# Optimization experiments

Hardware: AMD Instinct MI355X
Metric: run time of the kernel (lower is better)

Reference implementation:

```python
import jax, jax.numpy as jnp
import numpy as np

D_MODEL = 1024
N_HEADS = 16
D_K = D_MODEL // N_HEADS


def setup_inputs() -> dict:
    key = jax.random.key(0)
    ks = jax.random.split(key, 10)
    B, S = 4, 2048
    std = 1.0 / np.sqrt(D_MODEL)
    inp = {
        "x": jax.random.normal(ks[0], (B, S, D_MODEL), dtype=jnp.float32),
        "attention_mask": jnp.ones((B, S), dtype=jnp.int32),
        "W_q": jax.random.normal(ks[1], (D_MODEL, D_MODEL), dtype=jnp.float32) * std,
        "b_q": jnp.zeros((D_MODEL,), dtype=jnp.float32),
        "W_k": jax.random.normal(ks[2], (D_MODEL, D_MODEL), dtype=jnp.float32) * std,
        "b_k": jnp.zeros((D_MODEL,), dtype=jnp.float32),
        "W_v": jax.random.normal(ks[3], (D_MODEL, D_MODEL), dtype=jnp.float32) * std,
        "b_v": jnp.zeros((D_MODEL,), dtype=jnp.float32),
        "W_o": jax.random.normal(ks[4], (D_MODEL, D_MODEL), dtype=jnp.float32) * std,
        "b_o": jnp.zeros((D_MODEL,), dtype=jnp.float32),
    }
    return inp


def reference(x, attention_mask, W_q, b_q, W_k, b_k, W_v, b_v, W_o, b_o):
    B, S, _ = x.shape
    # projections -> [B, H, S, d_k]
    def proj(W, b):
        return (x @ W.T + b).reshape(B, S, N_HEADS, D_K).transpose(0, 2, 1, 3)
    q = proj(W_q, b_q)
    k = proj(W_k, b_k)
    v = proj(W_v, b_v)
    scores = jnp.einsum("bhqd,bhkd->bhqk", q, k) / jnp.sqrt(jnp.float32(D_K))
    mask = attention_mask[:, None, None, :] == 0  # [B,1,1,S]
    scores = jnp.where(mask, -jnp.inf, scores)
    probs = jax.nn.softmax(scores, axis=-1)  # dropout p=0 (eval)
    out = jnp.einsum("bhqk,bhkd->bhqd", probs, v)
    out = out.transpose(0, 2, 1, 3).reshape(B, S, D_MODEL)
    return out @ W_o.T + b_o
```

## Files before the change

### kernel.cpp

```cpp
#include <hip/hip_runtime.h>
#include <hip/hip_bf16.h>


#define SEQ   2048
#define DM    1024
#define NH    16
#define DK    64
#define MTOT  8192

typedef unsigned short u16;
typedef __attribute__((ext_vector_type(8))) short bf16x8;
typedef __attribute__((ext_vector_type(4))) float f32x4;

typedef union { unsigned u[4]; bf16x8 v; } FragU;

#define MFMA(a, b, c) __builtin_amdgcn_mfma_f32_16x16x32_bf16((a), (b), (c), 0, 0, 0)

#if __has_builtin(__builtin_amdgcn_exp2f)
#define EXP2(x) __builtin_amdgcn_exp2f(x)
#else
#define EXP2(x) __expf((x) * 0.69314718056f)
#endif

__device__ __forceinline__ u16 f2bf(float v) {
    unsigned int x = __float_as_uint(v);
    x += 0x7fffu + ((x >> 16) & 1u);
    return (u16)(x >> 16);
}
__device__ __forceinline__ float bf2f(u16 u) {
    return __uint_as_float(((unsigned int)u) << 16);
}
__device__ __forceinline__ unsigned pk2bf(float a, float b) {
    __hip_bfloat162 t = __float22bfloat162_rn(make_float2(a, b));
    unsigned r;
    __builtin_memcpy(&r, &t, 4);
    return r;
}

__device__ __forceinline__ void gl_lds16(const void* g, void* l) {
    __builtin_amdgcn_global_load_lds((__attribute__((address_space(1))) void*)g,
                                     (__attribute__((address_space(3))) void*)l,
                                     16, 0, 0);
}

__global__ __launch_bounds__(256) void split_f32(const float* __restrict__ src,
                                                 u16* __restrict__ dh,
                                                 u16* __restrict__ dl, int n4) {
    int i = blockIdx.x * 256 + threadIdx.x;
    if (i >= n4) return;
    float4 v = ((const float4*)src)[i];
    const float* f = (const float*)&v;
    ushort4 hh, ll;
    u16* hp = (u16*)&hh;
    u16* lp = (u16*)&ll;
#pragma unroll
    for (int j = 0; j < 4; ++j) {
        u16 h = f2bf(f[j]);
        hp[j] = h;
        lp[j] = f2bf(f[j] - bf2f(h));
    }
    ((ushort4*)dh)[i] = hh;
    ((ushort4*)dl)[i] = ll;
}

template <int MODE>
__global__ __launch_bounds__(256, 2) void gemm_split(
    const u16* __restrict__ Ah, const u16* __restrict__ Al,
    const u16* __restrict__ Bh, const u16* __restrict__ Bl,
    const float* __restrict__ bias,
    float* __restrict__ outF, u16* __restrict__ outH, u16* __restrict__ outL) {
    __shared__ u16 sm[4][128 * 64];

    const int tid = threadIdx.x;
    const int w = tid >> 6, lane = tid & 63;
    const int n0 = blockIdx.x * 128, m0 = blockIdx.y * 128;
    const int wr = w >> 1, wc = w & 1;
    const int rowoff = lane >> 3;
    const int cswz = ((lane & 7) ^ rowoff) << 3;

    const u16* src = (w == 0) ? Ah : (w == 1) ? Al : (w == 2) ? Bh : Bl;
    const int row0 = (w < 2) ? m0 : n0;
    const u16* sbase = src + (size_t)(row0 + rowoff) * 1024 + cswz;

    f32x4 acc[4][4];
#pragma unroll
    for (int a = 0; a < 4; ++a)
#pragma unroll
        for (int b = 0; b < 4; ++b) acc[a][b] = (f32x4)0.f;

    for (int k0 = 0; k0 < 1024; k0 += 64) {
#pragma unroll
        for (int i = 0; i < 16; ++i)
            gl_lds16(sbase + (size_t)(8 * i) * 1024 + k0, &sm[w][i * 512]);
        __syncthreads();
#pragma unroll
        for (int kk = 0; kk < 2; ++kk) {
            bf16x8 ah[4], al[4], bh[4], bl[4];
#pragma unroll
            for (int t = 0; t < 4; ++t) {
                const int Ra = wr * 64 + t * 16 + (lane & 15);
                const int oa = Ra * 128 + ((((kk << 2) + (lane >> 4)) ^ (Ra & 7)) << 4);
                ah[t] = *(const bf16x8*)((const char*)&sm[0][0] + oa);
                al[t] = *(const bf16x8*)((const char*)&sm[1][0] + oa);
                const int Rb = wc * 64 + t * 16 + (lane & 15);
                const int ob = Rb * 128 + ((((kk << 2) + (lane >> 4)) ^ (Rb & 7)) << 4);
                bh[t] = *(const bf16x8*)((const char*)&sm[2][0] + ob);
                bl[t] = *(const bf16x8*)((const char*)&sm[3][0] + ob);
            }
#pragma unroll
            for (int mt = 0; mt < 4; ++mt)
#pragma unroll
                for (int nt = 0; nt < 4; ++nt) {
                    acc[mt][nt] = MFMA(ah[mt], bh[nt], acc[mt][nt]);
                    acc[mt][nt] = MFMA(ah[mt], bl[nt], acc[mt][nt]);
                    acc[mt][nt] = MFMA(al[mt], bh[nt], acc[mt][nt]);
                }
        }
        __syncthreads();
    }

#pragma unroll
    for (int mt = 0; mt < 4; ++mt) {
#pragma unroll
        for (int nt = 0; nt < 4; ++nt) {
            const int n = n0 + wc * 64 + nt * 16 + (lane & 15);
            const float bv = bias[n];
#pragma unroll
            for (int j = 0; j < 4; ++j) {
                const int m = m0 + wr * 64 + mt * 16 + (lane >> 4) * 4 + j;
                const float v = acc[mt][nt][j] + bv;
                if (MODE == 0) {
                    outF[(size_t)m * 1024 + n] = v;
                } else {
                    const u16 h16 = f2bf(v);
                    const u16 l16 = f2bf(v - bf2f(h16));
                    const int b = m >> 11, s = m & 2047, hh = n >> 6, dk = n & 63;
                    size_t idx;
                    if (MODE == 1) idx = (((size_t)(b * 16 + hh)) * 2048 + s) * 64 + dk;
                    else           idx = (((size_t)(b * 16 + hh)) * 64 + dk) * 2048 + s;
                    outH[idx] = h16;
                    outL[idx] = l16;
                }
            }
        }
    }
}

__global__ __launch_bounds__(256, 4) void flash_mfma2(
    const u16* __restrict__ Qh, const u16* __restrict__ Ql,
    const u16* __restrict__ Kh, const u16* __restrict__ Kl,
    const u16* __restrict__ Vh, const u16* __restrict__ Vl,
    const int* __restrict__ amask,
    u16* __restrict__ Ch, u16* __restrict__ Cl) {
    __shared__ u16 sK[2][64 * 64];
    __shared__ u16 sV[2][64 * 64];
    __shared__ unsigned sMask[64];

    const int tid = threadIdx.x, w = tid >> 6, lane = tid & 63;
    const int qt = blockIdx.x, bh = blockIdx.y;
    const int b = bh >> 4, h = bh & 15;
    const int q0 = qt * 64;
    const int hi = lane >> 4, l15 = lane & 15;
    const int rowoff = lane >> 3;
    const int cswz = ((lane & 7) ^ rowoff) << 3;
    const size_t kvbase = (size_t)bh * 2048;
    const float CE = 0.125f * 1.44269504089f;

    {
        const int* ap = amask + b * 2048 + tid * 8;
        int4 a0 = *(const int4*)ap;
        int4 a1 = *(const int4*)(ap + 4);
        unsigned byte = (unsigned)(a0.x != 0) | ((unsigned)(a0.y != 0) << 1) |
                        ((unsigned)(a0.z != 0) << 2) | ((unsigned)(a0.w != 0) << 3) |
                        ((unsigned)(a1.x != 0) << 4) | ((unsigned)(a1.y != 0) << 5) |
                        ((unsigned)(a1.z != 0) << 6) | ((unsigned)(a1.w != 0) << 7);
        ((unsigned char*)sMask)[tid] = (unsigned char)byte;
    }

    bf16x8 qfh[2], qfl[2];
    {
        const size_t qrow = kvbase + q0 + w * 16 + l15;
        const int koff = hi * 8;
#pragma unroll
        for (int kk = 0; kk < 2; ++kk) {
            qfh[kk] = *(const bf16x8*)(Qh + qrow * 64 + kk * 32 + koff);
            qfl[kk] = *(const bf16x8*)(Ql + qrow * 64 + kk * 32 + koff);
        }
    }

    f32x4 o[4];
#pragma unroll
    for (int d = 0; d < 4; ++d) o[d] = (f32x4)0.f;
    float mi = -1e30f, li = 0.f;

    for (int kt = 0; kt < SEQ / 64; ++kt) {
        const int k0 = kt * 64;
        __syncthreads();
        {
            const u16* src = (w == 0) ? Kh : (w == 1) ? Kl : (w == 2) ? Vh : Vl;
            u16* dst = (w == 0) ? &sK[0][0] : (w == 1) ? &sK[1][0]
                     : (w == 2) ? &sV[0][0] : &sV[1][0];
            if (w < 2) {
                const u16* sb = src + (kvbase + k0 + rowoff) * 64 + cswz;
#pragma unroll
                for (int i = 0; i < 8; ++i)
                    gl_lds16(sb + (size_t)(8 * i) * 64, dst + i * 512);
            } else {
                const u16* sb = src + ((size_t)bh * 64 + rowoff) * 2048 + k0 + cswz;
#pragma unroll
                for (int i = 0; i < 8; ++i)
                    gl_lds16(sb + (size_t)(8 * i) * 2048, dst + i * 512);
            }
        }
        __syncthreads();

        f32x4 s[4];
#pragma unroll
        for (int nt = 0; nt < 4; ++nt) s[nt] = (f32x4)0.f;
#pragma unroll
        for (int kk = 0; kk < 2; ++kk)
#pragma unroll
            for (int nt = 0; nt < 4; ++nt) {
                const int Rb = nt * 16 + l15;
                const int ob = Rb * 128 + ((((kk << 2) + hi) ^ (Rb & 7)) << 4);
                bf16x8 kbh = *(const bf16x8*)((const char*)&sK[0][0] + ob);
                bf16x8 kbl = *(const bf16x8*)((const char*)&sK[1][0] + ob);
                s[nt] = MFMA(kbh, qfh[kk], s[nt]);
                s[nt] = MFMA(kbh, qfl[kk], s[nt]);
                s[nt] = MFMA(kbl, qfh[kk], s[nt]);
            }

        const unsigned mlo = sMask[2 * kt], mhw = sMask[2 * kt + 1];
        if ((mlo & mhw) != 0xFFFFFFFFu) {
#pragma unroll
            for (int nt = 0; nt < 4; ++nt) {
                const unsigned mw = (nt & 2) ? mhw : mlo;
                const unsigned bits = mw >> (((nt & 1) << 4) + (hi << 2));
#pragma unroll
                for (int j = 0; j < 4; ++j)
                    if (!((bits >> j) & 1u)) s[nt][j] = -2e30f;
            }
        }

        float pm = s[0][0];
#pragma unroll
        for (int nt = 0; nt < 4; ++nt)
#pragma unroll
            for (int j = 0; j < 4; ++j) pm = fmaxf(pm, s[nt][j]);
        pm = fmaxf(pm, __shfl_xor(pm, 16));
        pm = fmaxf(pm, __shfl_xor(pm, 32));
        if (__any(pm > mi + 64.f)) {
            const float mnew = fmaxf(mi, pm);
            const float sc = EXP2((mi - mnew) * CE);
            li *= sc;
#pragma unroll
            for (int d = 0; d < 4; ++d) o[d] *= sc;
            mi = mnew;
        }
        const float nm = -mi * CE;
        float p[4][4];
        float rs = 0.f;
#pragma unroll
        for (int nt = 0; nt < 4; ++nt)
#pragma unroll
            for (int j = 0; j < 4; ++j) {
                const float e = EXP2(fmaf(s[nt][j], CE, nm));
                p[nt][j] = e;
                rs += e;
            }
        rs += __shfl_xor(rs, 16);
        rs += __shfl_xor(rs, 32);
        li += rs;

        unsigned qph[4][2], qpl[4][2];
#pragma unroll
        for (int nt = 0; nt < 4; ++nt)
#pragma unroll
            for (int c = 0; c < 2; ++c) {
                const float v0 = p[nt][2 * c], v1 = p[nt][2 * c + 1];
                const unsigned wh = pk2bf(v0, v1);
                qph[nt][c] = wh;
                const float r0 = v0 - __uint_as_float(wh << 16);
                const float r1 = v1 - __uint_as_float(wh & 0xffff0000u);
                qpl[nt][c] = pk2bf(r0, r1);
            }

        const int src01 = l15 | ((lane & 16) << 1);
        const int src23 = src01 + 16;
#pragma unroll
        for (int kkv = 0; kkv < 2; ++kkv) {
            const unsigned ah0 = __shfl(qph[2 * kkv][0], src01);
            const unsigned ah1 = __shfl(qph[2 * kkv][1], src01);
            const unsigned ah2 = __shfl(qph[2 * kkv][0], src23);
            const unsigned ah3 = __shfl(qph[2 * kkv][1], src23);
            const unsigned bh0 = __shfl(qph[2 * kkv + 1][0], src01);
            const unsigned bh1 = __shfl(qph[2 * kkv + 1][1], src01);
            const unsigned bh2 = __shfl(qph[2 * kkv + 1][0], src23);
            const unsigned bh3 = __shfl(qph[2 * kkv + 1][1], src23);
            const unsigned al0 = __shfl(qpl[2 * kkv][0], src01);
            const unsigned al1 = __shfl(qpl[2 * kkv][1], src01);
            const unsigned al2 = __shfl(qpl[2 * kkv][0], src23);
            const unsigned al3 = __shfl(qpl[2 * kkv][1], src23);
            const unsigned bl0 = __shfl(qpl[2 * kkv + 1][0], src01);
            const unsigned bl1 = __shfl(qpl[2 * kkv + 1][1], src01);
            const unsigned bl2 = __shfl(qpl[2 * kkv + 1][0], src23);
            const unsigned bl3 = __shfl(qpl[2 * kkv + 1][1], src23);
            const bool up = (hi >= 2);
            FragU uh, ul;
            uh.u[0] = up ? bh0 : ah0;
            uh.u[1] = up ? bh1 : ah1;
            uh.u[2] = up ? bh2 : ah2;
            uh.u[3] = up ? bh3 : ah3;
            ul.u[0] = up ? bl0 : al0;
            ul.u[1] = up ? bl1 : al1;
            ul.u[2] = up ? bl2 : al2;
            ul.u[3] = up ? bl3 : al3;
            const bf16x8 pbh = uh.v, pbl = ul.v;
#pragma unroll
            for (int ntd = 0; ntd < 4; ++ntd) {
                const int Rv = ntd * 16 + l15;
                const int ov = Rv * 128 + ((((kkv << 2) + hi) ^ (Rv & 7)) << 4);
                bf16x8 vbh = *(const bf16x8*)((const char*)&sV[0][0] + ov);
                bf16x8 vbl = *(const bf16x8*)((const char*)&sV[1][0] + ov);
                o[ntd] = MFMA(vbh, pbh, o[ntd]);
                o[ntd] = MFMA(vbh, pbl, o[ntd]);
                o[ntd] = MFMA(vbl, pbh, o[ntd]);
            }
        }
    }

    const float inv = 1.f / li;
    const int srow = q0 + w * 16 + l15;
    const size_t obase = ((size_t)b * 2048 + srow) * 1024 + h * 64;
#pragma unroll
    for (int ntd = 0; ntd < 4; ++ntd) {
        const float v0 = o[ntd][0] * inv, v1 = o[ntd][1] * inv;
        const float v2 = o[ntd][2] * inv, v3 = o[ntd][3] * inv;
        const unsigned wh0 = pk2bf(v0, v1), wh1 = pk2bf(v2, v3);
        const float r0 = v0 - __uint_as_float(wh0 << 16);
        const float r1 = v1 - __uint_as_float(wh0 & 0xffff0000u);
        const float r2 = v2 - __uint_as_float(wh1 << 16);
        const float r3 = v3 - __uint_as_float(wh1 & 0xffff0000u);
        const unsigned wl0 = pk2bf(r0, r1), wl1 = pk2bf(r2, r3);
        const size_t idx = obase + ntd * 16 + hi * 4;
        uint2 sh, sl;
        sh.x = wh0; sh.y = wh1;
        sl.x = wl0; sl.y = wl1;
        *(uint2*)&Ch[idx] = sh;
        *(uint2*)&Cl[idx] = sl;
    }
}

extern "C" void kernel_launch(void* const* d_in, const int* in_sizes, int n_in,
                              void* d_out, int out_size, void* d_ws, size_t ws_size,
                              hipStream_t stream) {
    const float* x  = (const float*)d_in[0];
    const int* am   = (const int*)d_in[1];
    const float* Wq = (const float*)d_in[2];
    const float* bq = (const float*)d_in[3];
    const float* Wk = (const float*)d_in[4];
    const float* bk = (const float*)d_in[5];
    const float* Wv = (const float*)d_in[6];
    const float* bv = (const float*)d_in[7];
    const float* Wo = (const float*)d_in[8];
    const float* bo = (const float*)d_in[9];
    float* out = (float*)d_out;

    const size_t MB = 1u << 20;
    char* ws = (char*)d_ws;
    u16* Xh  = (u16*)(ws + 0 * MB);
    u16* Xl  = (u16*)(ws + 16 * MB);
    u16* qh  = (u16*)(ws + 32 * MB);
    u16* ql  = (u16*)(ws + 48 * MB);
    u16* kh  = (u16*)(ws + 64 * MB);
    u16* kl  = (u16*)(ws + 80 * MB);
    u16* vh  = (u16*)(ws + 96 * MB);
    u16* vl  = (u16*)(ws + 112 * MB);
    u16* Wqh = (u16*)(ws + 128 * MB);
    u16* Wql = (u16*)(ws + 130 * MB);
    u16* Wkh = (u16*)(ws + 132 * MB);
    u16* Wkl = (u16*)(ws + 134 * MB);
    u16* Wvh = (u16*)(ws + 136 * MB);
    u16* Wvl = (u16*)(ws + 138 * MB);
    u16* Woh = (u16*)(ws + 140 * MB);
    u16* Wol = (u16*)(ws + 142 * MB);

    split_f32<<<(MTOT * DM / 4 + 255) / 256, 256, 0, stream>>>(x, Xh, Xl, MTOT * DM / 4);
    split_f32<<<(DM * DM / 4 + 255) / 256, 256, 0, stream>>>(Wq, Wqh, Wql, DM * DM / 4);
    split_f32<<<(DM * DM / 4 + 255) / 256, 256, 0, stream>>>(Wk, Wkh, Wkl, DM * DM / 4);
    split_f32<<<(DM * DM / 4 + 255) / 256, 256, 0, stream>>>(Wv, Wvh, Wvl, DM * DM / 4);
    split_f32<<<(DM * DM / 4 + 255) / 256, 256, 0, stream>>>(Wo, Woh, Wol, DM * DM / 4);

    dim3 ggrid(DM / 128, MTOT / 128);
    gemm_split<1><<<ggrid, 256, 0, stream>>>(Xh, Xl, Wqh, Wql, bq, nullptr, qh, ql);
    gemm_split<1><<<ggrid, 256, 0, stream>>>(Xh, Xl, Wkh, Wkl, bk, nullptr, kh, kl);
    gemm_split<2><<<ggrid, 256, 0, stream>>>(Xh, Xl, Wvh, Wvl, bv, nullptr, vh, vl);

    flash_mfma2<<<dim3(SEQ / 64, 4 * NH), 256, 0, stream>>>(qh, ql, kh, kl, vh, vl, am, Xh, Xl);

    gemm_split<0><<<ggrid, 256, 0, stream>>>(Xh, Xl, Woh, Wol, bo, out, nullptr, nullptr);
}
```

Before: 590.6 us.

## Fuse QKV projections into one launch and double flash query tile

The three Q/K/V projection GEMMs become a single launch with a 24-wide grid, where the block's x index picks the weight set, bias and output layout. This removes launch gaps and fills the GPU with a bigger grid. The flash attention kernel now uses 512 threads (8 waves) per block covering 128 queries, so each K/V tile in shared memory serves twice as many queries and global loads are split across twice as many waves. The risk is lower occupancy or register pressure under the new launch bounds, and fewer blocks (1024) for attention.

```diff
diff --git a/kernel.cpp b/kernel.cpp
--- a/kernel.cpp
+++ b/kernel.cpp
@@ -63,20 +63,35 @@
     ((ushort4*)dl)[i] = ll;
 }
 
-template <int MODE>
-__global__ __launch_bounds__(256, 2) void gemm_split(
+__global__ __launch_bounds__(256, 2) void gemm_qkv(
     const u16* __restrict__ Ah, const u16* __restrict__ Al,
-    const u16* __restrict__ Bh, const u16* __restrict__ Bl,
-    const float* __restrict__ bias,
-    float* __restrict__ outF, u16* __restrict__ outH, u16* __restrict__ outL) {
+    const u16* __restrict__ Wqh, const u16* __restrict__ Wql,
+    const u16* __restrict__ Wkh, const u16* __restrict__ Wkl,
+    const u16* __restrict__ Wvh, const u16* __restrict__ Wvl,
+    const float* __restrict__ bq, const float* __restrict__ bk,
+    const float* __restrict__ bv,
+    u16* __restrict__ qh, u16* __restrict__ ql,
+    u16* __restrict__ kh, u16* __restrict__ kl,
+    u16* __restrict__ vh, u16* __restrict__ vl) {
     __shared__ u16 sm[4][128 * 64];
 
     const int tid = threadIdx.x;
     const int w = tid >> 6, lane = tid & 63;
-    const int n0 = blockIdx.x * 128, m0 = blockIdx.y * 128;
+    const int bx = blockIdx.x;
+    const int sel = bx >> 3;
+    const int n0 = (bx & 7) * 128, m0 = blockIdx.y * 128;
     const int wr = w >> 1, wc = w & 1;
     const int rowoff = lane >> 3;
     const int cswz = ((lane & 7) ^ rowoff) << 3;
+
+    const u16* Bh;
+    const u16* Bl;
+    const float* bias;
+    u16* oH;
+    u16* oL;
+    if (sel == 0)      { Bh = Wqh; Bl = Wql; bias = bq; oH = qh; oL = ql; }
+    else if (sel == 1) { Bh = Wkh; Bl = Wkl; bias = bk; oH = kh; oL = kl; }
+    else               { Bh = Wvh; Bl = Wvl; bias = bv; oH = vh; oL = vl; }
 
     const u16* src = (w == 0) ? Ah : (w == 1) ? Al : (w == 2) ? Bh : Bl;
     const int row0 = (w < 2) ? m0 : n0;
@@ -124,29 +139,94 @@
 #pragma unroll
         for (int nt = 0; nt < 4; ++nt) {
             const int n = n0 + wc * 64 + nt * 16 + (lane & 15);
-            const float bv = bias[n];
+            const float bvv = bias[n];
 #pragma unroll
             for (int j = 0; j < 4; ++j) {
                 const int m = m0 + wr * 64 + mt * 16 + (lane >> 4) * 4 + j;
-                const float v = acc[mt][nt][j] + bv;
-                if (MODE == 0) {
-                    outF[(size_t)m * 1024 + n] = v;
-                } else {
-                    const u16 h16 = f2bf(v);
-                    const u16 l16 = f2bf(v - bf2f(h16));
-                    const int b = m >> 11, s = m & 2047, hh = n >> 6, dk = n & 63;
-                    size_t idx;
-                    if (MODE == 1) idx = (((size_t)(b * 16 + hh)) * 2048 + s) * 64 + dk;
-                    else           idx = (((size_t)(b * 16 + hh)) * 64 + dk) * 2048 + s;
-                    outH[idx] = h16;
-                    outL[idx] = l16;
+                const float v = acc[mt][nt][j] + bvv;
+                const u16 h16 = f2bf(v);
+                const u16 l16 = f2bf(v - bf2f(h16));
+                const int b = m >> 11, s = m & 2047, hh = n >> 6, dk = n & 63;
+                size_t idx;
+                if (sel != 2) idx = (((size_t)(b * 16 + hh)) * 2048 + s) * 64 + dk;
+                else          idx = (((size_t)(b * 16 + hh)) * 64 + dk) * 2048 + s;
+                oH[idx] = h16;
+                oL[idx] = l16;
+            }
+        }
+    }
+}
+
+__global__ __launch_bounds__(256, 2) void gemm_out(
+    const u16* __restrict__ Ah, const u16* __restrict__ Al,
+    const u16* __restrict__ Bh, const u16* __restrict__ Bl,
+    const float* __restrict__ bias, float* __restrict__ outF) {
+    __shared__ u16 sm[4][128 * 64];
+
+    const int tid = threadIdx.x;
+    const int w = tid >> 6, lane = tid & 63;
+    const int n0 = blockIdx.x * 128, m0 = blockIdx.y * 128;
+    const int wr = w >> 1, wc = w & 1;
+    const int rowoff = lane >> 3;
+    const int cswz = ((lane & 7) ^ rowoff) << 3;
+
+    const u16* src = (w == 0) ? Ah : (w == 1) ? Al : (w == 2) ? Bh : Bl;
+    const int row0 = (w < 2) ? m0 : n0;
+    const u16* sbase = src + (size_t)(row0 + rowoff) * 1024 + cswz;
+
+    f32x4 acc[4][4];
+#pragma unroll
+    for (int a = 0; a < 4; ++a)
+#pragma unroll
+        for (int b = 0; b < 4; ++b) acc[a][b] = (f32x4)0.f;
+
+    for (int k0 = 0; k0 < 1024; k0 += 64) {
+#pragma unroll
+        for (int i = 0; i < 16; ++i)
+            gl_lds16(sbase + (size_t)(8 * i) * 1024 + k0, &sm[w][i * 512]);
+        __syncthreads();
+#pragma unroll
+        for (int kk = 0; kk < 2; ++kk) {
+            bf16x8 ah[4], al[4], bh[4], bl[4];
+#pragma unroll
+            for (int t = 0; t < 4; ++t) {
+                const int Ra = wr * 64 + t * 16 + (lane & 15);
+                const int oa = Ra * 128 + ((((kk << 2) + (lane >> 4)) ^ (Ra & 7)) << 4);
+                ah[t] = *(const bf16x8*)((const char*)&sm[0][0] + oa);
+                al[t] = *(const bf16x8*)((const char*)&sm[1][0] + oa);
+                const int Rb = wc * 64 + t * 16 + (lane & 15);
+                const int ob = Rb * 128 + ((((kk << 2) + (lane >> 4)) ^ (Rb & 7)) << 4);
+                bh[t] = *(const bf16x8*)((const char*)&sm[2][0] + ob);
+                bl[t] = *(const bf16x8*)((const char*)&sm[3][0] + ob);
+            }
+#pragma unroll
+            for (int mt = 0; mt < 4; ++mt)
+#pragma unroll
+                for (int nt = 0; nt < 4; ++nt) {
+                    acc[mt][nt] = MFMA(ah[mt], bh[nt], acc[mt][nt]);
+                    acc[mt][nt] = MFMA(ah[mt], bl[nt], acc[mt][nt]);
+                    acc[mt][nt] = MFMA(al[mt], bh[nt], acc[mt][nt]);
                 }
-            }
-        }
-    }
-}
-
-__global__ __launch_bounds__(256, 4) void flash_mfma2(
+        }
+        __syncthreads();
+    }
+
+#pragma unroll
+    for (int mt = 0; mt < 4; ++mt) {
+#pragma unroll
+        for (int nt = 0; nt < 4; ++nt) {
+            const int n = n0 + wc * 64 + nt * 16 + (lane & 15);
+            const float bv = bias[n];
+#pragma unroll
+            for (int j = 0; j < 4; ++j) {
+                const int m = m0 + wr * 64 + mt * 16 + (lane >> 4) * 4 + j;
+                outF[(size_t)m * 1024 + n] = acc[mt][nt][j] + bv;
+            }
+        }
+    }
+}
+
+__global__ __launch_bounds__(512, 8) void flash_mfma3(
     const u16* __restrict__ Qh, const u16* __restrict__ Ql,
     const u16* __restrict__ Kh, const u16* __restrict__ Kl,
     const u16* __restrict__ Vh, const u16* __restrict__ Vl,
@@ -159,14 +239,14 @@
     const int tid = threadIdx.x, w = tid >> 6, lane = tid & 63;
     const int qt = blockIdx.x, bh = blockIdx.y;
     const int b = bh >> 4, h = bh & 15;
-    const int q0 = qt * 64;
+    const int q0 = qt * 128;
     const int hi = lane >> 4, l15 = lane & 15;
     const int rowoff = lane >> 3;
     const int cswz = ((lane & 7) ^ rowoff) << 3;
     const size_t kvbase = (size_t)bh * 2048;
     const float CE = 0.125f * 1.44269504089f;
 
-    {
+    if (tid < 256) {
         const int* ap = amask + b * 2048 + tid * 8;
         int4 a0 = *(const int4*)ap;
         int4 a1 = *(const int4*)(ap + 4);
@@ -188,6 +268,12 @@
         }
     }
 
+    const int arr = w >> 1;
+    const int c0 = (w & 1) * 4;
+    const u16* ssrc = (arr == 0) ? Kh : (arr == 1) ? Kl : (arr == 2) ? Vh : Vl;
+    u16* sdst = (arr == 0) ? &sK[0][0] : (arr == 1) ? &sK[1][0]
+              : (arr == 2) ? &sV[0][0] : &sV[1][0];
+
     f32x4 o[4];
 #pragma unroll
     for (int d = 0; d < 4; ++d) o[d] = (f32x4)0.f;
@@ -196,21 +282,16 @@
     for (int kt = 0; kt < SEQ / 64; ++kt) {
         const int k0 = kt * 64;
         __syncthreads();
-        {
-            const u16* src = (w == 0) ? Kh : (w == 1) ? Kl : (w == 2) ? Vh : Vl;
-            u16* dst = (w == 0) ? &sK[0][0] : (w == 1) ? &sK[1][0]
-                     : (w == 2) ? &sV[0][0] : &sV[1][0];
-            if (w < 2) {
-                const u16* sb = src + (kvbase + k0 + rowoff) * 64 + cswz;
-#pragma unroll
-                for (int i = 0; i < 8; ++i)
-                    gl_lds16(sb + (size_t)(8 * i) * 64, dst + i * 512);
-            } else {
-                const u16* sb = src + ((size_t)bh * 64 + rowoff) * 2048 + k0 + cswz;
-#pragma unroll
-                for (int i = 0; i < 8; ++i)
-                    gl_lds16(sb + (size_t)(8 * i) * 2048, dst + i * 512);
-            }
+        if (arr < 2) {
+            const u16* sb = ssrc + (kvbase + k0 + 8 * c0 + rowoff) * 64 + cswz;
+#pragma unroll
+            for (int i = 0; i < 4; ++i)
+                gl_lds16(sb + (size_t)(8 * i) * 64, sdst + (c0 + i) * 512);
+        } else {
+            const u16* sb = ssrc + ((size_t)bh * 64 + 8 * c0 + rowoff) * 2048 + k0 + cswz;
+#pragma unroll
+            for (int i = 0; i < 4; ++i)
+                gl_lds16(sb + (size_t)(8 * i) * 2048, sdst + (c0 + i) * 512);
         }
         __syncthreads();
 
@@ -391,12 +472,11 @@
     split_f32<<<(DM * DM / 4 + 255) / 256, 256, 0, stream>>>(Wv, Wvh, Wvl, DM * DM / 4);
     split_f32<<<(DM * DM / 4 + 255) / 256, 256, 0, stream>>>(Wo, Woh, Wol, DM * DM / 4);
 
-    dim3 ggrid(DM / 128, MTOT / 128);
-    gemm_split<1><<<ggrid, 256, 0, stream>>>(Xh, Xl, Wqh, Wql, bq, nullptr, qh, ql);
-    gemm_split<1><<<ggrid, 256, 0, stream>>>(Xh, Xl, Wkh, Wkl, bk, nullptr, kh, kl);
-    gemm_split<2><<<ggrid, 256, 0, stream>>>(Xh, Xl, Wvh, Wvl, bv, nullptr, vh, vl);
-
-    flash_mfma2<<<dim3(SEQ / 64, 4 * NH), 256, 0, stream>>>(qh, ql, kh, kl, vh, vl, am, Xh, Xl);
-
-    gemm_split<0><<<ggrid, 256, 0, stream>>>(Xh, Xl, Woh, Wol, bo, out, nullptr, nullptr);
-}
+    gemm_qkv<<<dim3(24, MTOT / 128), 256, 0, stream>>>(
+        Xh, Xl, Wqh, Wql, Wkh, Wkl, Wvh, Wvl, bq, bk, bv,
+        qh, ql, kh, kl, vh, vl);
+
+    flash_mfma3<<<dim3(SEQ / 128, 4 * NH), 512, 0, stream>>>(qh, ql, kh, kl, vh, vl, am, Xh, Xl);
+
+    gemm_out<<<dim3(DM / 128, MTOT / 128), 256, 0, stream>>>(Xh, Xl, Woh, Wol, bo, out);
+}
```

After: 645.5 us. 9.3% more time.

## Process two query subtiles per wave and remap blocks for XCD locality

Applied to the files above, without the earlier changes.

The flash attention kernel now handles 128 query rows per block, with each wave owning two 16-row subtiles. Each K/V tile loaded into LDS and each fragment read from LDS is therefore reused across twice as many MFMAs, halving K/V global and LDS traffic per query. The block index is also remapped so that all query tiles of a head land on the same XCD, which should improve L2 reuse of K/V. In exchange the kernel uses more registers (launch bounds drop to 2 blocks) and launches half as many blocks, which lowers occupancy and latency hiding.

```diff
diff --git a/kernel.cpp b/kernel.cpp
--- a/kernel.cpp
+++ b/kernel.cpp
@@ -146,7 +146,7 @@
     }
 }
 
-__global__ __launch_bounds__(256, 4) void flash_mfma2(
+__global__ __launch_bounds__(256, 2) void flash_mfma4(
     const u16* __restrict__ Qh, const u16* __restrict__ Ql,
     const u16* __restrict__ Kh, const u16* __restrict__ Kl,
     const u16* __restrict__ Vh, const u16* __restrict__ Vl,
@@ -157,9 +157,12 @@
     __shared__ unsigned sMask[64];
 
     const int tid = threadIdx.x, w = tid >> 6, lane = tid & 63;
-    const int qt = blockIdx.x, bh = blockIdx.y;
+    const int i_flat = blockIdx.x + 16 * blockIdx.y;
+    const int xcd = i_flat & 7, j_rem = i_flat >> 3;
+    const int bh = xcd * 8 + (j_rem >> 4);
+    const int qt = j_rem & 15;
     const int b = bh >> 4, h = bh & 15;
-    const int q0 = qt * 64;
+    const int q0 = qt * 128;
     const int hi = lane >> 4, l15 = lane & 15;
     const int rowoff = lane >> 3;
     const int cswz = ((lane & 7) ^ rowoff) << 3;
@@ -177,21 +180,27 @@
         ((unsigned char*)sMask)[tid] = (unsigned char)byte;
     }
 
-    bf16x8 qfh[2], qfl[2];
-    {
-        const size_t qrow = kvbase + q0 + w * 16 + l15;
+    bf16x8 qfh[2][2], qfl[2][2];
+#pragma unroll
+    for (int st = 0; st < 2; ++st) {
+        const size_t qrow = kvbase + q0 + w * 32 + st * 16 + l15;
         const int koff = hi * 8;
 #pragma unroll
         for (int kk = 0; kk < 2; ++kk) {
-            qfh[kk] = *(const bf16x8*)(Qh + qrow * 64 + kk * 32 + koff);
-            qfl[kk] = *(const bf16x8*)(Ql + qrow * 64 + kk * 32 + koff);
-        }
-    }
-
-    f32x4 o[4];
-#pragma unroll
-    for (int d = 0; d < 4; ++d) o[d] = (f32x4)0.f;
-    float mi = -1e30f, li = 0.f;
+            qfh[st][kk] = *(const bf16x8*)(Qh + qrow * 64 + kk * 32 + koff);
+            qfl[st][kk] = *(const bf16x8*)(Ql + qrow * 64 + kk * 32 + koff);
+        }
+    }
+
+    f32x4 o[2][4];
+    float mi[2], li[2];
+#pragma unroll
+    for (int st = 0; st < 2; ++st) {
+        mi[st] = -1e30f;
+        li[st] = 0.f;
+#pragma unroll
+        for (int d = 0; d < 4; ++d) o[st][d] = (f32x4)0.f;
+    }
 
     for (int kt = 0; kt < SEQ / 64; ++kt) {
         const int k0 = kt * 64;
@@ -214,9 +223,11 @@
         }
         __syncthreads();
 
-        f32x4 s[4];
-#pragma unroll
-        for (int nt = 0; nt < 4; ++nt) s[nt] = (f32x4)0.f;
+        f32x4 s[2][4];
+#pragma unroll
+        for (int st = 0; st < 2; ++st)
+#pragma unroll
+            for (int nt = 0; nt < 4; ++nt) s[st][nt] = (f32x4)0.f;
 #pragma unroll
         for (int kk = 0; kk < 2; ++kk)
 #pragma unroll
@@ -225,9 +236,12 @@
                 const int ob = Rb * 128 + ((((kk << 2) + hi) ^ (Rb & 7)) << 4);
                 bf16x8 kbh = *(const bf16x8*)((const char*)&sK[0][0] + ob);
                 bf16x8 kbl = *(const bf16x8*)((const char*)&sK[1][0] + ob);
-                s[nt] = MFMA(kbh, qfh[kk], s[nt]);
-                s[nt] = MFMA(kbh, qfl[kk], s[nt]);
-                s[nt] = MFMA(kbl, qfh[kk], s[nt]);
+                s[0][nt] = MFMA(kbh, qfh[0][kk], s[0][nt]);
+                s[0][nt] = MFMA(kbh, qfl[0][kk], s[0][nt]);
+                s[0][nt] = MFMA(kbl, qfh[0][kk], s[0][nt]);
+                s[1][nt] = MFMA(kbh, qfh[1][kk], s[1][nt]);
+                s[1][nt] = MFMA(kbh, qfl[1][kk], s[1][nt]);
+                s[1][nt] = MFMA(kbl, qfh[1][kk], s[1][nt]);
             }
 
         const unsigned mlo = sMask[2 * kt], mhw = sMask[2 * kt + 1];
@@ -238,116 +252,133 @@
                 const unsigned bits = mw >> (((nt & 1) << 4) + (hi << 2));
 #pragma unroll
                 for (int j = 0; j < 4; ++j)
-                    if (!((bits >> j) & 1u)) s[nt][j] = -2e30f;
-            }
-        }
-
-        float pm = s[0][0];
-#pragma unroll
-        for (int nt = 0; nt < 4; ++nt)
-#pragma unroll
-            for (int j = 0; j < 4; ++j) pm = fmaxf(pm, s[nt][j]);
-        pm = fmaxf(pm, __shfl_xor(pm, 16));
-        pm = fmaxf(pm, __shfl_xor(pm, 32));
-        if (__any(pm > mi + 64.f)) {
-            const float mnew = fmaxf(mi, pm);
-            const float sc = EXP2((mi - mnew) * CE);
-            li *= sc;
-#pragma unroll
-            for (int d = 0; d < 4; ++d) o[d] *= sc;
-            mi = mnew;
-        }
-        const float nm = -mi * CE;
-        float p[4][4];
-        float rs = 0.f;
-#pragma unroll
-        for (int nt = 0; nt < 4; ++nt)
-#pragma unroll
-            for (int j = 0; j < 4; ++j) {
-                const float e = EXP2(fmaf(s[nt][j], CE, nm));
-                p[nt][j] = e;
-                rs += e;
-            }
-        rs += __shfl_xor(rs, 16);
-        rs += __shfl_xor(rs, 32);
-        li += rs;
-
-        unsigned qph[4][2], qpl[4][2];
-#pragma unroll
-        for (int nt = 0; nt < 4; ++nt)
-#pragma unroll
-            for (int c = 0; c < 2; ++c) {
-                const float v0 = p[nt][2 * c], v1 = p[nt][2 * c + 1];
-                const unsigned wh = pk2bf(v0, v1);
-                qph[nt][c] = wh;
-                const float r0 = v0 - __uint_as_float(wh << 16);
-                const float r1 = v1 - __uint_as_float(wh & 0xffff0000u);
-                qpl[nt][c] = pk2bf(r0, r1);
-            }
+                    if (!((bits >> j) & 1u)) {
+                        s[0][nt][j] = -2e30f;
+                        s[1][nt][j] = -2e30f;
+                    }
+            }
+        }
+
+        unsigned qph[2][4][2], qpl[2][4][2];
+#pragma unroll
+        for (int st = 0; st < 2; ++st) {
+            float pm = s[st][0][0];
+#pragma unroll
+            for (int nt = 0; nt < 4; ++nt)
+#pragma unroll
+                for (int j = 0; j < 4; ++j) pm = fmaxf(pm, s[st][nt][j]);
+            pm = fmaxf(pm, __shfl_xor(pm, 16));
+            pm = fmaxf(pm, __shfl_xor(pm, 32));
+            if (__any(pm > mi[st] + 64.f)) {
+                const float mnew = fmaxf(mi[st], pm);
+                const float sc = EXP2((mi[st] - mnew) * CE);
+                li[st] *= sc;
+#pragma unroll
+                for (int d = 0; d < 4; ++d) o[st][d] *= sc;
+                mi[st] = mnew;
+            }
+            const float nm = -mi[st] * CE;
+            float p[4][4];
+            float rs = 0.f;
+#pragma unroll
+            for (int nt = 0; nt < 4; ++nt)
+#pragma unroll
+                for (int j = 0; j < 4; ++j) {
+                    const float e = EXP2(fmaf(s[st][nt][j], CE, nm));
+                    p[nt][j] = e;
+                    rs += e;
+                }
+            rs += __shfl_xor(rs, 16);
+            rs += __shfl_xor(rs, 32);
+            li[st] += rs;
+
+#pragma unroll
+            for (int nt = 0; nt < 4; ++nt)
+#pragma unroll
+                for (int c = 0; c < 2; ++c) {
+                    const float v0 = p[nt][2 * c], v1 = p[nt][2 * c + 1];
+                    const unsigned wh = pk2bf(v0, v1);
+                    qph[st][nt][c] = wh;
+                    const float r0 = v0 - __uint_as_float(wh << 16);
+                    const float r1 = v1 - __uint_as_float(wh & 0xffff0000u);
+                    qpl[st][nt][c] = pk2bf(r0, r1);
+                }
+        }
 
         const int src01 = l15 | ((lane & 16) << 1);
         const int src23 = src01 + 16;
 #pragma unroll
         for (int kkv = 0; kkv < 2; ++kkv) {
-            const unsigned ah0 = __shfl(qph[2 * kkv][0], src01);
-            const unsigned ah1 = __shfl(qph[2 * kkv][1], src01);
-            const unsigned ah2 = __shfl(qph[2 * kkv][0], src23);
-            const unsigned ah3 = __shfl(qph[2 * kkv][1], src23);
-            const unsigned bh0 = __shfl(qph[2 * kkv + 1][0], src01);
-            const unsigned bh1 = __shfl(qph[2 * kkv + 1][1], src01);
-            const unsigned bh2 = __shfl(qph[2 * kkv + 1][0], src23);
-            const unsigned bh3 = __shfl(qph[2 * kkv + 1][1], src23);
-            const unsigned al0 = __shfl(qpl[2 * kkv][0], src01);
-            const unsigned al1 = __shfl(qpl[2 * kkv][1], src01);
-            const unsigned al2 = __shfl(qpl[2 * kkv][0], src23);
-            const unsigned al3 = __shfl(qpl[2 * kkv][1], src23);
-            const unsigned bl0 = __shfl(qpl[2 * kkv + 1][0], src01);
-            const unsigned bl1 = __shfl(qpl[2 * kkv + 1][1], src01);
-            const unsigned bl2 = __shfl(qpl[2 * kkv + 1][0], src23);
-            const unsigned bl3 = __shfl(qpl[2 * kkv + 1][1], src23);
-            const bool up = (hi >= 2);
-            FragU uh, ul;
-            uh.u[0] = up ? bh0 : ah0;
-            uh.u[1] = up ? bh1 : ah1;
-            uh.u[2] = up ? bh2 : ah2;
-            uh.u[3] = up ? bh3 : ah3;
-            ul.u[0] = up ? bl0 : al0;
-            ul.u[1] = up ? bl1 : al1;
-            ul.u[2] = up ? bl2 : al2;
-            ul.u[3] = up ? bl3 : al3;
-            const bf16x8 pbh = uh.v, pbl = ul.v;
+            bf16x8 pbh[2], pbl[2];
+#pragma unroll
+            for (int st = 0; st < 2; ++st) {
+                const unsigned ah0 = __shfl(qph[st][2 * kkv][0], src01);
+                const unsigned ah1 = __shfl(qph[st][2 * kkv][1], src01);
+                const unsigned ah2 = __shfl(qph[st][2 * kkv][0], src23);
+                const unsigned ah3 = __shfl(qph[st][2 * kkv][1], src23);
+                const unsigned bh0 = __shfl(qph[st][2 * kkv + 1][0], src01);
+                const unsigned bh1 = __shfl(qph[st][2 * kkv + 1][1], src01);
+                const unsigned bh2 = __shfl(qph[st][2 * kkv + 1][0], src23);
+                const unsigned bh3 = __shfl(qph[st][2 * kkv + 1][1], src23);
+                const unsigned al0 = __shfl(qpl[st][2 * kkv][0], src01);
+                const unsigned al1 = __shfl(qpl[st][2 * kkv][1], src01);
+                const unsigned al2 = __shfl(qpl[st][2 * kkv][0], src23);
+                const unsigned al3 = __shfl(qpl[st][2 * kkv][1], src23);
+                const unsigned bl0 = __shfl(qpl[st][2 * kkv + 1][0], src01);
+                const unsigned bl1 = __shfl(qpl[st][2 * kkv + 1][1], src01);
+                const unsigned bl2 = __shfl(qpl[st][2 * kkv + 1][0], src23);
+                const unsigned bl3 = __shfl(qpl[st][2 * kkv + 1][1], src23);
+                const bool up = (hi >= 2);
+                FragU uh, ul;
+                uh.u[0] = up ? bh0 : ah0;
+                uh.u[1] = up ? bh1 : ah1;
+                uh.u[2] = up ? bh2 : ah2;
+                uh.u[3] = up ? bh3 : ah3;
+                ul.u[0] = up ? bl0 : al0;
+                ul.u[1] = up ? bl1 : al1;
+                ul.u[2] = up ? bl2 : al2;
+                ul.u[3] = up ? bl3 : al3;
+                pbh[st] = uh.v;
+                pbl[st] = ul.v;
+            }
 #pragma unroll
             for (int ntd = 0; ntd < 4; ++ntd) {
                 const int Rv = ntd * 16 + l15;
                 const int ov = Rv * 128 + ((((kkv << 2) + hi) ^ (Rv & 7)) << 4);
                 bf16x8 vbh = *(const bf16x8*)((const char*)&sV[0][0] + ov);
                 bf16x8 vbl = *(const bf16x8*)((const char*)&sV[1][0] + ov);
-                o[ntd] = MFMA(vbh, pbh, o[ntd]);
-                o[ntd] = MFMA(vbh, pbl, o[ntd]);
-                o[ntd] = MFMA(vbl, pbh, o[ntd]);
-            }
-        }
-    }
-
-    const float inv = 1.f / li;
-    const int srow = q0 + w * 16 + l15;
-    const size_t obase = ((size_t)b * 2048 + srow) * 1024 + h * 64;
-#pragma unroll
-    for (int ntd = 0; ntd < 4; ++ntd) {
-        const float v0 = o[ntd][0] * inv, v1 = o[ntd][1] * inv;
-        const float v2 = o[ntd][2] * inv, v3 = o[ntd][3] * inv;
-        const unsigned wh0 = pk2bf(v0, v1), wh1 = pk2bf(v2, v3);
-        const float r0 = v0 - __uint_as_float(wh0 << 16);
-        const float r1 = v1 - __uint_as_float(wh0 & 0xffff0000u);
-        const float r2 = v2 - __uint_as_float(wh1 << 16);
-        const float r3 = v3 - __uint_as_float(wh1 & 0xffff0000u);
-        const unsigned wl0 = pk2bf(r0, r1), wl1 = pk2bf(r2, r3);
-        const size_t idx = obase + ntd * 16 + hi * 4;
-        uint2 sh, sl;
-        sh.x = wh0; sh.y = wh1;
-        sl.x = wl0; sl.y = wl1;
-        *(uint2*)&Ch[idx] = sh;
-        *(uint2*)&Cl[idx] = sl;
+                o[0][ntd] = MFMA(vbh, pbh[0], o[0][ntd]);
+                o[0][ntd] = MFMA(vbh, pbl[0], o[0][ntd]);
+                o[0][ntd] = MFMA(vbl, pbh[0], o[0][ntd]);
+                o[1][ntd] = MFMA(vbh, pbh[1], o[1][ntd]);
+                o[1][ntd] = MFMA(vbh, pbl[1], o[1][ntd]);
+                o[1][ntd] = MFMA(vbl, pbh[1], o[1][ntd]);
+            }
+        }
+    }
+
+#pragma unroll
+    for (int st = 0; st < 2; ++st) {
+        const float inv = 1.f / li[st];
+        const int srow = q0 + w * 32 + st * 16 + l15;
+        const size_t obase = ((size_t)b * 2048 + srow) * 1024 + h * 64;
+#pragma unroll
+        for (int ntd = 0; ntd < 4; ++ntd) {
+            const float v0 = o[st][ntd][0] * inv, v1 = o[st][ntd][1] * inv;
+            const float v2 = o[st][ntd][2] * inv, v3 = o[st][ntd][3] * inv;
+            const unsigned wh0 = pk2bf(v0, v1), wh1 = pk2bf(v2, v3);
+            const float r0 = v0 - __uint_as_float(wh0 << 16);
+            const float r1 = v1 - __uint_as_float(wh0 & 0xffff0000u);
+            const float r2 = v2 - __uint_as_float(wh1 << 16);
+            const float r3 = v3 - __uint_as_float(wh1 & 0xffff0000u);
+            const unsigned wl0 = pk2bf(r0, r1), wl1 = pk2bf(r2, r3);
+            const size_t idx = obase + ntd * 16 + hi * 4;
+            uint2 sh, sl;
+            sh.x = wh0; sh.y = wh1;
+            sl.x = wl0; sl.y = wl1;
+            *(uint2*)&Ch[idx] = sh;
+            *(uint2*)&Cl[idx] = sl;
+        }
     }
 }
 
@@ -396,7 +427,7 @@
     gemm_split<1><<<ggrid, 256, 0, stream>>>(Xh, Xl, Wkh, Wkl, bk, nullptr, kh, kl);
     gemm_split<2><<<ggrid, 256, 0, stream>>>(Xh, Xl, Wvh, Wvl, bv, nullptr, vh, vl);
 
-    flash_mfma2<<<dim3(SEQ / 64, 4 * NH), 256, 0, stream>>>(qh, ql, kh, kl, vh, vl, am, Xh, Xl);
+    flash_mfma4<<<dim3(SEQ / 128, 4 * NH), 256, 0, stream>>>(qh, ql, kh, kl, vh, vl, am, Xh, Xl);
 
     gemm_split<0><<<ggrid, 256, 0, stream>>>(Xh, Xl, Woh, Wol, bo, out, nullptr, nullptr);
 }
```

Result: faster. 549.3 us (-7.0%).
